# Optimization experiments

Measured on AMD Instinct MI355X. Metric: run time of the kernel, lower is better.

## Reference

```python
import jax, jax.numpy as jnp
import numpy as np

CH = 512
HEADS = 4
GROUPS = 32  # _groups(512) -> 32
EPS = 1e-5


def setup_inputs() -> dict:
    key = jax.random.key(0)
    ks = jax.random.split(key, 7)
    b, c, h, w = 16, CH, 32, 32
    sd = 1.0 / np.sqrt(c)
    return {
        "x": jax.random.normal(ks[0], (b, c, h, w), dtype=jnp.float32),
        "gamma": jnp.ones((c,), jnp.float32),
        "beta": jnp.zeros((c,), jnp.float32),
        "w_qkv": jax.random.normal(ks[1], (3 * c, c), dtype=jnp.float32) * sd,
        "b_qkv": jax.random.normal(ks[2], (3 * c,), dtype=jnp.float32) * 0.01,
        "w_proj": jax.random.normal(ks[3], (c, c), dtype=jnp.float32) * sd,
        "b_proj": jax.random.normal(ks[4], (c,), dtype=jnp.float32) * 0.01,
    }


def _group_norm(x, gamma, beta):
    b, c, h, w = x.shape
    xg = x.reshape(b, GROUPS, -1)  # (b, G, c//G * h * w)
    mu = jnp.mean(xg, axis=-1, keepdims=True)
    var = jnp.var(xg, axis=-1, keepdims=True)
    xn = ((xg - mu) * jax.lax.rsqrt(var + EPS)).reshape(b, c, h, w)
    return xn * gamma[None, :, None, None] + beta[None, :, None, None]


def reference(x, gamma, beta, w_qkv, b_qkv, w_proj, b_proj):
    b, c, h, w = x.shape
    hd = c // HEADS
    xn = _group_norm(x, gamma, beta)
    # 1x1 conv == channel matmul
    qkv = jnp.einsum('oc,bchw->bohw', w_qkv, xn) + b_qkv[None, :, None, None]
    qkv = qkv.reshape(b, 3, HEADS, hd, h * w)
    q, k, v = qkv[:, 0], qkv[:, 1], qkv[:, 2]  # (b, H, hd, n)
    scale = hd ** -0.5
    attn = jax.nn.softmax(jnp.einsum('bhcn,bhcm->bhnm', q * scale, k), axis=-1)
    out = jnp.einsum('bhnm,bhcm->bhcn', attn, v).reshape(b, c, h, w)
    out = jnp.einsum('oc,bchw->bohw', w_proj, out) + b_proj[None, :, None, None]
    return x + out
```

## Files before the change

### kernel.cpp

```cpp
#include <hip/hip_runtime.h>

#define CH 512
#define HEADS 4
#define HD 128
#define NPIX 1024
#define BATCH 16
#define GROUPS 32
#define GSZ 16
#define EPS 1e-5f

typedef _Float16 f16;
typedef _Float16 f16x8 __attribute__((ext_vector_type(8)));
typedef _Float16 f16x4 __attribute__((ext_vector_type(4)));
typedef float f32x4 __attribute__((ext_vector_type(4)));

__device__ __forceinline__ void gld16(const f16* g, f16* l) {
    __builtin_amdgcn_global_load_lds((__attribute__((address_space(1))) const void*)g,
                                     (__attribute__((address_space(3))) void*)l, 16, 0, 0);
}

__global__ void k_convert(const float* __restrict__ wq, const float* __restrict__ wp,
                          f16* __restrict__ wqT, f16* __restrict__ wpT) {
    int c = blockIdx.x * 256 + threadIdx.x;
    {
        int ot = c >> 13, kbl = (c >> 7) & 63, ol = c & 127;
        const float* s = wq + ((size_t)(ot * 128 + ol)) * CH + kbl * 8;
        f32x4 a = *(const f32x4*)s, b = *(const f32x4*)(s + 4);
        f16x8 v;
        v[0] = (f16)a.x; v[1] = (f16)a.y; v[2] = (f16)a.z; v[3] = (f16)a.w;
        v[4] = (f16)b.x; v[5] = (f16)b.y; v[6] = (f16)b.z; v[7] = (f16)b.w;
        *(f16x8*)(wqT + (size_t)c * 8) = v;
    }
    if (c < 32768) {
        int ot = c >> 13, kbl = (c >> 7) & 63, ol = c & 127;
        const float* s = wp + ((size_t)(ot * 128 + ol)) * CH + kbl * 8;
        f32x4 a = *(const f32x4*)s, b = *(const f32x4*)(s + 4);
        f16x8 v;
        v[0] = (f16)a.x; v[1] = (f16)a.y; v[2] = (f16)a.z; v[3] = (f16)a.w;
        v[4] = (f16)b.x; v[5] = (f16)b.y; v[6] = (f16)b.z; v[7] = (f16)b.w;
        *(f16x8*)(wpT + (size_t)c * 8) = v;
    }
}

__global__ void k_stats(const float* __restrict__ x, float2* __restrict__ stats) {
    int bg = blockIdx.x;
    const f32x4* b4 = (const f32x4*)(x + (size_t)bg * (GSZ * NPIX));
    float s = 0.f, ss = 0.f;
    for (int i = threadIdx.x; i < GSZ * NPIX / 4; i += 256) {
        f32x4 v = b4[i];
        s  += v.x + v.y + v.z + v.w;
        ss += v.x * v.x + v.y * v.y + v.z * v.z + v.w * v.w;
    }
    for (int off = 32; off; off >>= 1) { s += __shfl_down(s, off); ss += __shfl_down(ss, off); }
    __shared__ float as_[4], ass[4];
    int wv = threadIdx.x >> 6, ln = threadIdx.x & 63;
    if (ln == 0) { as_[wv] = s; ass[wv] = ss; }
    __syncthreads();
    if (threadIdx.x == 0) {
        float S = as_[0] + as_[1] + as_[2] + as_[3];
        float SS = ass[0] + ass[1] + ass[2] + ass[3];
        float mu = S / (GSZ * NPIX);
        float var = SS / (GSZ * NPIX) - mu * mu;
        stats[bg] = make_float2(mu, rsqrtf(var + EPS));
    }
}

__global__ void k_norm_t(const float* __restrict__ x, const float* __restrict__ gamma,
                         const float* __restrict__ beta, const float2* __restrict__ stats,
                         f16* __restrict__ xnT) {
    int nt = blockIdx.x, ch = blockIdx.y, b = blockIdx.z;
    int t = threadIdx.x;
    int nl = (t & 31) * 4;
    int cl = (t >> 5) * 8;
    f16* tb = xnT + ((size_t)(b * 8 + nt)) * 65536;
#pragma unroll
    for (int it = 0; it < 4; it++) {
        int c8 = ch * 256 + it * 64 + cl;
        float2 stv = stats[b * GROUPS + (c8 >> 4)];
        f32x4 ga = *(const f32x4*)(gamma + c8), gb = *(const f32x4*)(gamma + c8 + 4);
        f32x4 ba = *(const f32x4*)(beta + c8),  bb = *(const f32x4*)(beta + c8 + 4);
        float gs[8] = {ga.x, ga.y, ga.z, ga.w, gb.x, gb.y, gb.z, gb.w};
        float bs[8] = {ba.x, ba.y, ba.z, ba.w, bb.x, bb.y, bb.z, bb.w};
#pragma unroll
        for (int i = 0; i < 8; i++) { gs[i] *= stv.y; bs[i] = bs[i] - stv.x * gs[i]; }
        f16x4 h[8];
#pragma unroll
        for (int i = 0; i < 8; i++) {
            f32x4 v = *(const f32x4*)(x + ((size_t)(b * CH + c8 + i)) * NPIX + nt * 128 + nl);
            h[i][0] = (f16)(v.x * gs[i] + bs[i]);
            h[i][1] = (f16)(v.y * gs[i] + bs[i]);
            h[i][2] = (f16)(v.z * gs[i] + bs[i]);
            h[i][3] = (f16)(v.w * gs[i] + bs[i]);
        }
#pragma unroll
        for (int j = 0; j < 4; j++) {
            f16x8 o_;
#pragma unroll
            for (int i = 0; i < 8; i++) o_[i] = h[i][j];
            *(f16x8*)(tb + (size_t)(c8 >> 3) * 1024 + (nl + j) * 8) = o_;
        }
    }
}

__global__ __launch_bounds__(256, 3) void k_qkv(const f16* __restrict__ wT, const float* __restrict__ bias,
                                                const f16* __restrict__ xnT, f16* __restrict__ qF,
                                                f16* __restrict__ kTl, f16* __restrict__ vTl) {
    int nt = blockIdx.x, ot = blockIdx.y, b = blockIdx.z;
    int o0 = ot * 128;
    __shared__ union SM {
        struct { f16 As[8192]; f16 Bs[8192]; } s;
        f16 Cf[16384];
    } sm;
    __shared__ float biasS[128];
    if (threadIdx.x < 128) biasS[threadIdx.x] = bias[o0 + threadIdx.x];
    int tid = threadIdx.x, lane = tid & 63, wv = tid >> 6;
    int wr = wv >> 1, wc = wv & 1;
    int l15 = lane & 15, quad = lane >> 4;
    const f16* wA = wT + (size_t)ot * 65536;
    const f16* xB = xnT + ((size_t)(b * 8 + nt)) * 65536;
    f32x4 acc[4][4] = {};
    for (int kk = 0; kk < CH; kk += 64) {
        __syncthreads();
        const f16* sa = wA + (size_t)(kk >> 3) * 1024;
        const f16* sb = xB + (size_t)(kk >> 3) * 1024;
#pragma unroll
        for (int i = 0; i < 4; i++) {
            int s = wv * 4 + i;
            gld16(sa + (size_t)(s * 64 + lane) * 8, sm.s.As + s * 512);
            gld16(sb + (size_t)(s * 64 + lane) * 8, sm.s.Bs + s * 512);
        }
        __syncthreads();
#pragma unroll
        for (int dk = 0; dk < 2; dk++) {
            f16x8 af[4], bf[4];
#pragma unroll
            for (int t = 0; t < 4; t++) {
                af[t] = *(const f16x8*)(sm.s.As + (dk * 4 + quad) * 1024 + (wr * 64 + t * 16 + l15) * 8);
                bf[t] = *(const f16x8*)(sm.s.Bs + (dk * 4 + quad) * 1024 + (wc * 64 + t * 16 + l15) * 8);
            }
#pragma unroll
            for (int tm = 0; tm < 4; tm++)
#pragma unroll
                for (int tn = 0; tn < 4; tn++)
                    acc[tm][tn] = __builtin_amdgcn_mfma_f32_16x16x32_f16(af[tm], bf[tn], acc[tm][tn], 0, 0, 0);
        }
    }
    __syncthreads();
    int which = ot >> 2, h = ot & 3;
#pragma unroll
    for (int tm = 0; tm < 4; tm++)
#pragma unroll
        for (int tn = 0; tn < 4; tn++) {
            int ob = wr * 64 + tm * 16 + quad * 4;
            int n  = wc * 64 + tn * 16 + l15;
            f16x4 pv;
#pragma unroll
            for (int r = 0; r < 4; r++) pv[r] = (f16)(acc[tm][tn][r] + biasS[ob + r]);
            if (which == 0) {
                int addr = ((((n >> 5) * 2 + ((n >> 4) & 1)) * 4 + (ob >> 5)) * 512)
                         + ((ob >> 3) & 3) * 128 + (n & 15) * 8 + (quad & 1) * 4;
                *(f16x4*)&sm.Cf[addr] = pv;
            } else if (which == 1) {
                int addr = (ob >> 3) * 1024 + n * 8 + (quad & 1) * 4;
                *(f16x4*)&sm.Cf[addr] = pv;
            } else {
#pragma unroll
                for (int r = 0; r < 4; r++)
                    sm.Cf[(n >> 3) * 1024 + (ob + r) * 8 + (n & 7)] = pv[r];
            }
        }
    __syncthreads();
    f16* tb = (which == 0) ? (qF + ((size_t)((b * 4 + h) * 8 + nt)) * 16384)
            : (which == 1) ? (kTl + ((size_t)((b * 4 + h) * 8 + nt)) * 16384)
                           : (vTl + ((size_t)((b * 4 + h) * 8 + nt)) * 16384);
#pragma unroll
    for (int i = 0; i < 8; i++) {
        int cid = tid + i * 256;
        *(f16x8*)(tb + (size_t)cid * 8) = *(const f16x8*)(sm.Cf + cid * 8);
    }
}

__global__ __launch_bounds__(512, 1) void k_attn(const f16* __restrict__ qF, const f16* __restrict__ kTl,
                                                 const f16* __restrict__ vTl, f16* __restrict__ oT) {
    int bid = blockIdx.x;
    int ntp = bid >> 6, group = bid & 63;
    int b = group >> 2, h = group & 3;
    extern __shared__ f16 smem[];
    f16* Kl = smem;
    f16* Vl = smem + 16384;
    f16* PA = smem + 32768;
    f16* PB = smem + 49152;
    int tid = threadIdx.x, lane = tid & 63, wv = tid >> 6;
    int wq = wv & 3;
    int tile = wv >> 2;
    int nt = ntp * 2 + tile;
    int l15 = lane & 15, quad = lane >> 4;
    const f16* qb = qF + ((size_t)(group * 8 + nt)) * 16384;
    const f16* kb = kTl + (size_t)group * 8 * 16384;
    const f16* vb = vTl + (size_t)group * 8 * 16384;
    f16* Preg = tile ? PB : PA;

    f16x8 aq[2][4];
#pragma unroll
    for (int t = 0; t < 2; t++)
#pragma unroll
        for (int dk = 0; dk < 4; dk++) {
            int seg = (wq * 2 + t) * 4 + dk;
            f16x8 v = *(const f16x8*)(qb + seg * 512 + lane * 8);
            aq[t][dk] = v * (f16)0.08838834764831845f;
        }

    float m_i[2] = {-1e30f, -1e30f}, l_i[2] = {0.f, 0.f};
    f32x4 oaccT[2][8] = {};

    const f16* sbase = tile ? vb : kb;
    f16* dstL = tile ? Vl : Kl;
    f16x8 buf[8];
#pragma unroll
    for (int i = 0; i < 8; i++)
        buf[i] = *(const f16x8*)(sbase + (size_t)((wq * 8 + i) * 64 + lane) * 8);

    for (int mc = 0; mc < 8; mc++) {
        __syncthreads();
#pragma unroll
        for (int i = 0; i < 8; i++)
            *(f16x8*)&dstL[(wq * 8 + i) * 512 + lane * 8] = buf[i];
        __syncthreads();

        f32x4 st[2][8] = {};
#pragma unroll
        for (int dk = 0; dk < 4; dk++) {
            f16x8 kf[8];
#pragma unroll
            for (int t = 0; t < 8; t++)
                kf[t] = *(const f16x8*)&Kl[(dk * 4 + quad) * 1024 + (t * 16 + l15) * 8];
#pragma unroll
            for (int tr = 0; tr < 2; tr++)
#pragma unroll
                for (int tc = 0; tc < 8; tc++)
                    st[tr][tc] = __builtin_amdgcn_mfma_f32_16x16x32_f16(kf[tc], aq[tr][dk], st[tr][tc], 0, 0, 0);
        }

#pragma unroll
        for (int tr = 0; tr < 2; tr++) {
            float a[8];
#pragma unroll
            for (int tc = 0; tc < 8; tc++)
                a[tc] = fmaxf(fmaxf(st[tr][tc][0], st[tr][tc][1]), fmaxf(st[tr][tc][2], st[tr][tc][3]));
#pragma unroll
            for (int s = 4; s; s >>= 1)
#pragma unroll
                for (int k = 0; k < 4; k++) if (k < s) a[k] = fmaxf(a[k], a[k + s]);
            float mx = a[0];
            mx = fmaxf(mx, __shfl_xor(mx, 16));
            mx = fmaxf(mx, __shfl_xor(mx, 32));
            float mnew = fmaxf(m_i[tr], mx);
            float alpha = __expf(m_i[tr] - mnew);
            m_i[tr] = mnew;
            float r4[8];
#pragma unroll
            for (int tc = 0; tc < 8; tc++) {
                float p0 = __expf(st[tr][tc][0] - mnew);
                float p1 = __expf(st[tr][tc][1] - mnew);
                float p2 = __expf(st[tr][tc][2] - mnew);
                float p3 = __expf(st[tr][tc][3] - mnew);
                st[tr][tc][0] = p0; st[tr][tc][1] = p1;
                st[tr][tc][2] = p2; st[tr][tc][3] = p3;
                r4[tc] = (p0 + p1) + (p2 + p3);
            }
#pragma unroll
            for (int s = 4; s; s >>= 1)
#pragma unroll
                for (int k = 0; k < 4; k++) if (k < s) r4[k] += r4[k + s];
            float rs = r4[0];
            rs += __shfl_xor(rs, 16);
            rs += __shfl_xor(rs, 32);
            l_i[tr] = l_i[tr] * alpha + rs;
#pragma unroll
            for (int tc = 0; tc < 8; tc++) {
                oaccT[tr][tc].x *= alpha; oaccT[tr][tc].y *= alpha;
                oaccT[tr][tc].z *= alpha; oaccT[tr][tc].w *= alpha;
            }
        }

#pragma unroll
        for (int tr = 0; tr < 2; tr++) {
            int n = wq * 32 + tr * 16 + l15;
#pragma unroll
            for (int tc = 0; tc < 8; tc++) {
                int blk = tc * 2 + (quad >> 1);
                f16x4 pv;
#pragma unroll
                for (int r = 0; r < 4; r++) pv[r] = (f16)st[tr][tc][r];
                *(f16x4*)&Preg[n * 128 + ((blk ^ (n & 15)) << 3) + ((quad & 1) << 2)] = pv;
            }
        }

        if (mc < 7) {
            const f16* s = sbase + (size_t)(mc + 1) * 16384;
#pragma unroll
            for (int i = 0; i < 8; i++)
                buf[i] = *(const f16x8*)(s + (size_t)((wq * 8 + i) * 64 + lane) * 8);
        }

#pragma unroll
        for (int mk = 0; mk < 4; mk++) {
            f16x8 vf[8], pf[2];
#pragma unroll
            for (int t = 0; t < 8; t++)
                vf[t] = *(const f16x8*)&Vl[(mk * 4 + quad) * 1024 + (t * 16 + l15) * 8];
#pragma unroll
            for (int tr = 0; tr < 2; tr++) {
                int n = wq * 32 + tr * 16 + l15;
                int blk = mk * 4 + quad;
                pf[tr] = *(const f16x8*)&Preg[n * 128 + ((blk ^ (n & 15)) << 3)];
            }
#pragma unroll
            for (int tr = 0; tr < 2; tr++)
#pragma unroll
                for (int tc = 0; tc < 8; tc++)
                    oaccT[tr][tc] = __builtin_amdgcn_mfma_f32_16x16x32_f16(vf[tc], pf[tr], oaccT[tr][tc], 0, 0, 0);
        }
    }

#pragma unroll
    for (int tr = 0; tr < 2; tr++) {
        float inv = 1.f / l_i[tr];
        int n = wq * 32 + tr * 16 + l15;
#pragma unroll
        for (int tc = 0; tc < 8; tc++) {
            int blk = tc * 2 + (quad >> 1);
            f16x4 ov;
#pragma unroll
            for (int r = 0; r < 4; r++) ov[r] = (f16)(oaccT[tr][tc][r] * inv);
            *(f16x4*)&Preg[n * 128 + ((blk ^ (n & 15)) << 3) + ((quad & 1) << 2)] = ov;
        }
    }
    __syncthreads();
    f16* ob = oT + ((size_t)(b * 8 + nt)) * 65536;
    int t256 = tid & 255;
#pragma unroll
    for (int i = 0; i < 8; i++) {
        int cid = t256 + i * 256;
        int cbl = cid >> 7, n = cid & 127;
        f16x8 v = *(const f16x8*)&Preg[n * 128 + ((cbl ^ (n & 15)) << 3)];
        *(f16x8*)(ob + (size_t)(h * 16 + cbl) * 1024 + n * 8) = v;
    }
}

__global__ __launch_bounds__(256, 3) void k_proj(const f16* __restrict__ wT, const float* __restrict__ bias,
                                                 const f16* __restrict__ oT, const float* __restrict__ x,
                                                 float* __restrict__ out) {
    int nt = blockIdx.x, ot = blockIdx.y, b = blockIdx.z;
    int n0 = nt * 128, o0 = ot * 128;
    __shared__ union SM {
        struct { f16 As[8192]; f16 Bs[8192]; } s;
        f16 Cs[128][136];
    } sm;
    __shared__ float biasS[128];
    if (threadIdx.x < 128) biasS[threadIdx.x] = bias[o0 + threadIdx.x];
    int tid = threadIdx.x, lane = tid & 63, wv = tid >> 6;
    int wr = wv >> 1, wc = wv & 1;
    int l15 = lane & 15, quad = lane >> 4;
    const f16* wA = wT + (size_t)ot * 65536;
    const f16* xB = oT + ((size_t)(b * 8 + nt)) * 65536;
    f32x4 acc[4][4] = {};
    for (int kk = 0; kk < CH; kk += 64) {
        __syncthreads();
        const f16* sa = wA + (size_t)(kk >> 3) * 1024;
        const f16* sb = xB + (size_t)(kk >> 3) * 1024;
#pragma unroll
        for (int i = 0; i < 4; i++) {
            int s = wv * 4 + i;
            gld16(sa + (size_t)(s * 64 + lane) * 8, sm.s.As + s * 512);
            gld16(sb + (size_t)(s * 64 + lane) * 8, sm.s.Bs + s * 512);
        }
        __syncthreads();
#pragma unroll
        for (int dk = 0; dk < 2; dk++) {
            f16x8 af[4], bf[4];
#pragma unroll
            for (int t = 0; t < 4; t++) {
                af[t] = *(const f16x8*)(sm.s.As + (dk * 4 + quad) * 1024 + (wr * 64 + t * 16 + l15) * 8);
                bf[t] = *(const f16x8*)(sm.s.Bs + (dk * 4 + quad) * 1024 + (wc * 64 + t * 16 + l15) * 8);
            }
#pragma unroll
            for (int tm = 0; tm < 4; tm++)
#pragma unroll
                for (int tn = 0; tn < 4; tn++)
                    acc[tm][tn] = __builtin_amdgcn_mfma_f32_16x16x32_f16(af[tm], bf[tn], acc[tm][tn], 0, 0, 0);
        }
    }
    __syncthreads();
#pragma unroll
    for (int tm = 0; tm < 4; tm++)
#pragma unroll
        for (int tn = 0; tn < 4; tn++)
#pragma unroll
            for (int r = 0; r < 4; r++) {
                int o = wr * 64 + tm * 16 + quad * 4 + r;
                int n = wc * 64 + tn * 16 + l15;
                sm.Cs[o][n] = (f16)(acc[tm][tn][r] + biasS[o]);
            }
    __syncthreads();
#pragma unroll
    for (int i = 0; i < 8; i++) {
        int cid = tid + i * 256;
        int row = cid >> 4, off = (cid & 15) * 8;
        f16x8 v = *(const f16x8*)&sm.Cs[row][off];
        size_t gofs = ((size_t)(b * CH) + o0 + row) * NPIX + n0 + off;
        const float* xp = x + gofs;
        float* op = out + gofs;
        f32x4 o0v, o1v;
        o0v.x = xp[0] + (float)v[0]; o0v.y = xp[1] + (float)v[1];
        o0v.z = xp[2] + (float)v[2]; o0v.w = xp[3] + (float)v[3];
        o1v.x = xp[4] + (float)v[4]; o1v.y = xp[5] + (float)v[5];
        o1v.z = xp[6] + (float)v[6]; o1v.w = xp[7] + (float)v[7];
        *(f32x4*)op = o0v; *(f32x4*)(op + 4) = o1v;
    }
}

extern "C" void kernel_launch(void* const* d_in, const int* in_sizes, int n_in,
                              void* d_out, int out_size, void* d_ws, size_t ws_size,
                              hipStream_t stream) {
    const float* x     = (const float*)d_in[0];
    const float* gamma = (const float*)d_in[1];
    const float* beta  = (const float*)d_in[2];
    const float* wqkv  = (const float*)d_in[3];
    const float* bqkv  = (const float*)d_in[4];
    const float* wproj = (const float*)d_in[5];
    const float* bproj = (const float*)d_in[6];
    float* out = (float*)d_out;

    char* p = (char*)d_ws;
    float2* stats = (float2*)p;   p += 16 * 32 * sizeof(float2);
    f16* wqT = (f16*)p;           p += (size_t)3 * CH * CH * 2;
    f16* wpT = (f16*)p;           p += (size_t)CH * CH * 2;
    f16* xnT = (f16*)p;           p += (size_t)BATCH * NPIX * CH * 2;
    f16* qF  = (f16*)p;           p += (size_t)BATCH * HEADS * NPIX * HD * 2;
    f16* kTl = (f16*)p;           p += (size_t)BATCH * HEADS * NPIX * HD * 2;
    f16* vTl = (f16*)p;           p += (size_t)BATCH * HEADS * NPIX * HD * 2;
    f16* oT  = (f16*)p;           p += (size_t)BATCH * NPIX * CH * 2;

    k_convert<<<dim3(384), 256, 0, stream>>>(wqkv, wproj, wqT, wpT);
    k_stats<<<dim3(BATCH * GROUPS), 256, 0, stream>>>(x, stats);
    k_norm_t<<<dim3(8, 2, BATCH), 256, 0, stream>>>(x, gamma, beta, stats, xnT);
    k_qkv<<<dim3(8, 12, BATCH), 256, 0, stream>>>(wqT, bqkv, xnT, qF, kTl, vTl);

    hipFuncSetAttribute((const void*)k_attn, hipFuncAttributeMaxDynamicSharedMemorySize, 131072);
    k_attn<<<dim3(256), 512, 131072, stream>>>(qF, kTl, vTl, oT);

    k_proj<<<dim3(8, 4, BATCH), 256, 0, stream>>>(wpT, bproj, oT, x, out);
}
```

Baseline: 222.6 us.

## Fuse group-norm stats and normalize via LDS; exp2 softmax; earlier K/V prefetch

```diff
diff --git a/kernel.cpp b/kernel.cpp
--- a/kernel.cpp
+++ b/kernel.cpp
@@ -42,63 +42,50 @@
     }
 }
 
-__global__ void k_stats(const float* __restrict__ x, float2* __restrict__ stats) {
-    int bg = blockIdx.x;
-    const f32x4* b4 = (const f32x4*)(x + (size_t)bg * (GSZ * NPIX));
+__global__ __launch_bounds__(256, 2) void k_gn(const float* __restrict__ x, const float* __restrict__ gamma,
+                                               const float* __restrict__ beta, f16* __restrict__ xnT) {
+    int g = blockIdx.x, b = blockIdx.y;
+    __shared__ float xs[GSZ * NPIX];
+    __shared__ float red[8];
+    __shared__ float stat2[2];
+    const f32x4* x4 = (const f32x4*)(x + ((size_t)(b * GROUPS + g)) * (GSZ * NPIX));
     float s = 0.f, ss = 0.f;
     for (int i = threadIdx.x; i < GSZ * NPIX / 4; i += 256) {
-        f32x4 v = b4[i];
+        f32x4 v = x4[i];
+        *(f32x4*)&xs[i * 4] = v;
         s  += v.x + v.y + v.z + v.w;
         ss += v.x * v.x + v.y * v.y + v.z * v.z + v.w * v.w;
     }
     for (int off = 32; off; off >>= 1) { s += __shfl_down(s, off); ss += __shfl_down(ss, off); }
-    __shared__ float as_[4], ass[4];
     int wv = threadIdx.x >> 6, ln = threadIdx.x & 63;
-    if (ln == 0) { as_[wv] = s; ass[wv] = ss; }
+    if (ln == 0) { red[wv] = s; red[4 + wv] = ss; }
     __syncthreads();
     if (threadIdx.x == 0) {
-        float S = as_[0] + as_[1] + as_[2] + as_[3];
-        float SS = ass[0] + ass[1] + ass[2] + ass[3];
+        float S = red[0] + red[1] + red[2] + red[3];
+        float SS = red[4] + red[5] + red[6] + red[7];
         float mu = S / (GSZ * NPIX);
         float var = SS / (GSZ * NPIX) - mu * mu;
-        stats[bg] = make_float2(mu, rsqrtf(var + EPS));
-    }
-}
-
-__global__ void k_norm_t(const float* __restrict__ x, const float* __restrict__ gamma,
-                         const float* __restrict__ beta, const float2* __restrict__ stats,
-                         f16* __restrict__ xnT) {
-    int nt = blockIdx.x, ch = blockIdx.y, b = blockIdx.z;
-    int t = threadIdx.x;
-    int nl = (t & 31) * 4;
-    int cl = (t >> 5) * 8;
-    f16* tb = xnT + ((size_t)(b * 8 + nt)) * 65536;
-#pragma unroll
-    for (int it = 0; it < 4; it++) {
-        int c8 = ch * 256 + it * 64 + cl;
-        float2 stv = stats[b * GROUPS + (c8 >> 4)];
-        f32x4 ga = *(const f32x4*)(gamma + c8), gb = *(const f32x4*)(gamma + c8 + 4);
-        f32x4 ba = *(const f32x4*)(beta + c8),  bb = *(const f32x4*)(beta + c8 + 4);
-        float gs[8] = {ga.x, ga.y, ga.z, ga.w, gb.x, gb.y, gb.z, gb.w};
-        float bs[8] = {ba.x, ba.y, ba.z, ba.w, bb.x, bb.y, bb.z, bb.w};
-#pragma unroll
-        for (int i = 0; i < 8; i++) { gs[i] *= stv.y; bs[i] = bs[i] - stv.x * gs[i]; }
-        f16x4 h[8];
-#pragma unroll
-        for (int i = 0; i < 8; i++) {
-            f32x4 v = *(const f32x4*)(x + ((size_t)(b * CH + c8 + i)) * NPIX + nt * 128 + nl);
-            h[i][0] = (f16)(v.x * gs[i] + bs[i]);
-            h[i][1] = (f16)(v.y * gs[i] + bs[i]);
-            h[i][2] = (f16)(v.z * gs[i] + bs[i]);
-            h[i][3] = (f16)(v.w * gs[i] + bs[i]);
-        }
-#pragma unroll
-        for (int j = 0; j < 4; j++) {
-            f16x8 o_;
-#pragma unroll
-            for (int i = 0; i < 8; i++) o_[i] = h[i][j];
-            *(f16x8*)(tb + (size_t)(c8 >> 3) * 1024 + (nl + j) * 8) = o_;
-        }
+        stat2[0] = mu; stat2[1] = rsqrtf(var + EPS);
+    }
+    __syncthreads();
+    float mu = stat2[0], rstd = stat2[1];
+    int ch = threadIdx.x >> 7;
+    int n  = threadIdx.x & 127;
+    float gl[8], bl[8];
+#pragma unroll
+    for (int i = 0; i < 8; i++) {
+        float gv = gamma[g * 16 + ch * 8 + i] * rstd;
+        gl[i] = gv;
+        bl[i] = beta[g * 16 + ch * 8 + i] - mu * gv;
+    }
+    f16* tb0 = xnT + ((size_t)(b * 8)) * 65536 + (g * 2 + ch) * 1024 + n * 8;
+#pragma unroll
+    for (int nt = 0; nt < 8; nt++) {
+        f16x8 o;
+#pragma unroll
+        for (int i = 0; i < 8; i++)
+            o[i] = (f16)(xs[(ch * 8 + i) * 1024 + nt * 128 + n] * gl[i] + bl[i]);
+        *(f16x8*)(tb0 + (size_t)nt * 65536) = o;
     }
 }
 
@@ -207,7 +194,7 @@
         for (int dk = 0; dk < 4; dk++) {
             int seg = (wq * 2 + t) * 4 + dk;
             f16x8 v = *(const f16x8*)(qb + seg * 512 + lane * 8);
-            aq[t][dk] = v * (f16)0.08838834764831845f;
+            aq[t][dk] = v * (f16)0.12752961f;
         }
 
     float m_i[2] = {-1e30f, -1e30f}, l_i[2] = {0.f, 0.f};
@@ -226,6 +213,13 @@
         for (int i = 0; i < 8; i++)
             *(f16x8*)&dstL[(wq * 8 + i) * 512 + lane * 8] = buf[i];
         __syncthreads();
+
+        if (mc < 7) {
+            const f16* s = sbase + (size_t)(mc + 1) * 16384;
+#pragma unroll
+            for (int i = 0; i < 8; i++)
+                buf[i] = *(const f16x8*)(s + (size_t)((wq * 8 + i) * 64 + lane) * 8);
+        }
 
         f32x4 st[2][8] = {};
 #pragma unroll
@@ -255,15 +249,15 @@
             mx = fmaxf(mx, __shfl_xor(mx, 16));
             mx = fmaxf(mx, __shfl_xor(mx, 32));
             float mnew = fmaxf(m_i[tr], mx);
-            float alpha = __expf(m_i[tr] - mnew);
+            float alpha = exp2f(m_i[tr] - mnew);
             m_i[tr] = mnew;
             float r4[8];
 #pragma unroll
             for (int tc = 0; tc < 8; tc++) {
-                float p0 = __expf(st[tr][tc][0] - mnew);
-                float p1 = __expf(st[tr][tc][1] - mnew);
-                float p2 = __expf(st[tr][tc][2] - mnew);
-                float p3 = __expf(st[tr][tc][3] - mnew);
+                float p0 = exp2f(st[tr][tc][0] - mnew);
+                float p1 = exp2f(st[tr][tc][1] - mnew);
+                float p2 = exp2f(st[tr][tc][2] - mnew);
+                float p3 = exp2f(st[tr][tc][3] - mnew);
                 st[tr][tc][0] = p0; st[tr][tc][1] = p1;
                 st[tr][tc][2] = p2; st[tr][tc][3] = p3;
                 r4[tc] = (p0 + p1) + (p2 + p3);
@@ -294,13 +288,6 @@
                 for (int r = 0; r < 4; r++) pv[r] = (f16)st[tr][tc][r];
                 *(f16x4*)&Preg[n * 128 + ((blk ^ (n & 15)) << 3) + ((quad & 1) << 2)] = pv;
             }
-        }
-
-        if (mc < 7) {
-            const f16* s = sbase + (size_t)(mc + 1) * 16384;
-#pragma unroll
-            for (int i = 0; i < 8; i++)
-                buf[i] = *(const f16x8*)(s + (size_t)((wq * 8 + i) * 64 + lane) * 8);
         }
 
 #pragma unroll
@@ -433,7 +420,6 @@
     float* out = (float*)d_out;
 
     char* p = (char*)d_ws;
-    float2* stats = (float2*)p;   p += 16 * 32 * sizeof(float2);
     f16* wqT = (f16*)p;           p += (size_t)3 * CH * CH * 2;
     f16* wpT = (f16*)p;           p += (size_t)CH * CH * 2;
     f16* xnT = (f16*)p;           p += (size_t)BATCH * NPIX * CH * 2;
@@ -443,8 +429,7 @@
     f16* oT  = (f16*)p;           p += (size_t)BATCH * NPIX * CH * 2;
 
     k_convert<<<dim3(384), 256, 0, stream>>>(wqkv, wproj, wqT, wpT);
-    k_stats<<<dim3(BATCH * GROUPS), 256, 0, stream>>>(x, stats);
-    k_norm_t<<<dim3(8, 2, BATCH), 256, 0, stream>>>(x, gamma, beta, stats, xnT);
+    k_gn<<<dim3(GROUPS, BATCH), 256, 0, stream>>>(x, gamma, beta, xnT);
     k_qkv<<<dim3(8, 12, BATCH), 256, 0, stream>>>(wqT, bqkv, xnT, qF, kTl, vTl);
 
     hipFuncSetAttribute((const void*)k_attn, hipFuncAttributeMaxDynamicSharedMemorySize, 131072);
```

After: 246.5 us. 10.7% more time.
